# Kernel tuning notes

Measured on AMD Instinct MI355X. Metric: run time of the kernel, lower is better.

The kernel has to match this reference:

```python
import jax, jax.numpy as jnp
import numpy as np

BETA = 0.25  # cfg.vq_commitment


def setup_inputs() -> dict:
    key = jax.random.key(0)
    k1, k2 = jax.random.split(key)
    residual = jax.random.normal(k1, (16, 2048, 512), dtype=jnp.float32)
    emb_weight = jax.random.normal(k2, (1024, 512), dtype=jnp.float32) * 0.02
    return {"residual": residual, "emb_weight": emb_weight}


def reference(residual, emb_weight):
    # Euclidean branch (vq_cosine=False), no factorized projection (rvq_code_dim<=0)
    r = residual                                     # [B, T, D]
    z2 = jnp.sum(r * r, axis=-1, keepdims=True)      # [B, T, 1]
    e2 = jnp.sum(emb_weight * emb_weight, axis=-1)   # [N]
    # dist[b,t,n] = ||r_bt||^2 + ||e_n||^2 - 2 <r_bt, e_n>
    dist = z2 + e2 - 2.0 * jnp.einsum('btd,nd->btn', r, emb_weight)
    idx = jnp.argmin(dist, axis=-1)                  # [B, T] int
    z_q = emb_weight[idx]                            # gather, [B, T, D]
    # straight-through estimator
    z_st = residual + jax.lax.stop_gradient(z_q - residual)
    commit = jnp.mean((jax.lax.stop_gradient(z_q) - residual) ** 2)
    codebook = jnp.mean((z_q - jax.lax.stop_gradient(residual)) ** 2)
    loss = BETA * commit + codebook
    return (z_st, loss, dist, idx)
```

## Files before the change

### kernel.cpp

```cpp
#include <hip/hip_runtime.h>
#include <cfloat>
#include <stdint.h>

#define D       512
#define NCODES  1024
#define MROWS   32768

#define ZST_OFF  0
#define LOSS_OFF 16777216
#define DIST_OFF 16777217ull
#define IDX_OFF  50331649

#define WS_Z2   524288
#define WS_E2   557056
#define WS_LOSS 558080

typedef __attribute__((ext_vector_type(4))) float f32x4;
typedef __attribute__((ext_vector_type(4))) int   i32x4;
typedef __bf16 bf16v8 __attribute__((ext_vector_type(8)));

static __device__ __forceinline__ uint32_t f2bf(float x) {
    uint32_t u = __float_as_uint(x);
    return (u + 0x7fffu + ((u >> 16) & 1u)) >> 16;
}
static __device__ __forceinline__ float bf2f(uint32_t h) {
    return __uint_as_float(h << 16);
}
static __device__ __forceinline__ f32x4 MFMA(bf16v8 a, bf16v8 b, f32x4 c) {
    return __builtin_amdgcn_mfma_f32_16x16x32_bf16(a, b, c, 0, 0, 0);
}

__global__ void prepass_kernel(const float* __restrict__ residual,
                               const float* __restrict__ emb,
                               float* __restrict__ ws,
                               float* __restrict__ out) {
    if (blockIdx.x == 0 && threadIdx.x == 0) ws[WS_LOSS] = 0.0f;
    const int gwave = (int)((blockIdx.x * blockDim.x + threadIdx.x) >> 6);
    const int lane  = threadIdx.x & 63;
    const bool isA  = gwave < MROWS;
    const float* src = isA ? residual + (size_t)gwave * D
                           : emb + (size_t)(gwave - MROWS) * D;
    const float4* vp = (const float4*)src;
    float4 x0 = vp[lane * 2];
    float4 x1 = vp[lane * 2 + 1];
    float xs[8] = {x0.x, x0.y, x0.z, x0.w, x1.x, x1.y, x1.z, x1.w};
    uint32_t hp[4], lp[4];
    float s = 0.f;
#pragma unroll
    for (int i = 0; i < 4; ++i) {
        float a = xs[2 * i], b = xs[2 * i + 1];
        s += a * a + b * b;
        uint32_t h0 = f2bf(a), h1 = f2bf(b);
        uint32_t l0 = f2bf(a - bf2f(h0)), l1 = f2bf(b - bf2f(h1));
        hp[i] = h0 | (h1 << 16);
        lp[i] = l0 | (l1 << 16);
    }
#pragma unroll
    for (int off = 32; off > 0; off >>= 1) s += __shfl_xor(s, off);

    const int kt = lane >> 3, c8 = lane & 7;
    i32x4 hv = {(int)hp[0], (int)hp[1], (int)hp[2], (int)hp[3]};
    i32x4 lv = {(int)lp[0], (int)lp[1], (int)lp[2], (int)lp[3]};
    if (isA) {
        const int bm = gwave >> 7, rl = gwave & 127;
        char* dst = (char*)out + (size_t)bm * 262144 + (size_t)kt * 32768
                  + rl * 128 + ((c8 * 16) ^ ((rl & 7) << 4));
        *(i32x4*)dst = hv;
        *(i32x4*)(dst + 16384) = lv;
        if (lane == 0) ws[WS_Z2 + gwave] = s;
    } else {
        const int n = gwave - MROWS, nt = n >> 8, cl = n & 255;
        char* dst = (char*)ws + (size_t)nt * 524288 + (size_t)kt * 65536
                  + cl * 128 + ((c8 * 16) ^ ((cl & 7) << 4));
        *(i32x4*)dst = hv;
        *(i32x4*)(dst + 32768) = lv;
        if (lane == 0) ws[WS_E2 + n] = s;
    }
}

__launch_bounds__(512, 2)
__global__ void vq_main_kernel(const float* __restrict__ residual,
                               const float* __restrict__ emb,
                               float* __restrict__ ws,
                               float* __restrict__ out) {
    __shared__ __align__(16) char smem[98304];
    const int tid  = threadIdx.x;
    const int wid  = tid >> 6, lane = tid & 63;
    const int ln15 = lane & 15, kg = lane >> 4;
    const int wm   = wid >> 2, wn = wid & 3;
    const int bm   = blockIdx.x;
    const int row0 = bm * 128;

    float z2r[16];
#pragma unroll
    for (int mf = 0; mf < 4; ++mf)
#pragma unroll
        for (int j = 0; j < 4; ++j)
            z2r[mf * 4 + j] = ws[WS_Z2 + row0 + wm * 64 + mf * 16 + kg * 4 + j];

    float runv[16];
    int   runi[16];
#pragma unroll
    for (int li = 0; li < 16; ++li) { runv[li] = FLT_MAX; runi[li] = 0; }

    int aoff[4][2], boff[4][2];
#pragma unroll
    for (int mf = 0; mf < 4; ++mf) {
        const int rA = wm * 64 + mf * 16 + ln15;
#pragma unroll
        for (int ks = 0; ks < 2; ++ks)
            aoff[mf][ks] = rA * 128 + ((ks * 64 + kg * 16) ^ ((rA & 7) << 4));
    }
#pragma unroll
    for (int nf = 0; nf < 4; ++nf) {
        const int cB = wn * 64 + nf * 16 + ln15;
#pragma unroll
        for (int ks = 0; ks < 2; ++ks)
            boff[nf][ks] = 32768 + cB * 128 + ((ks * 64 + kg * 16) ^ ((cB & 7) << 4));
    }

    const char* srcA = (const char*)out + (size_t)bm * 262144;
    const char* srcB = (const char*)ws;

    for (int nt = 0; nt < 4; ++nt) {
        f32x4 acc[4][4];
#pragma unroll
        for (int mf = 0; mf < 4; ++mf)
#pragma unroll
            for (int nf = 0; nf < 4; ++nf) acc[mf][nf] = 0.f;

        for (int kt = 0; kt < 8; ++kt) {
            __syncthreads();
            {
                const char* ga = srcA + (size_t)kt * 32768 + wid * 1024 + lane * 16;
                char* la = smem + wid * 1024;
#pragma unroll
                for (int i = 0; i < 4; ++i)
                    __builtin_amdgcn_global_load_lds((const uint32_t*)(ga + i * 8192),
                                                     (uint32_t*)(la + i * 8192), 16, 0, 0);
                const char* gb = srcB + (size_t)nt * 524288 + (size_t)kt * 65536
                               + wid * 1024 + lane * 16;
                char* lb = smem + 32768 + wid * 1024;
#pragma unroll
                for (int i = 0; i < 8; ++i)
                    __builtin_amdgcn_global_load_lds((const uint32_t*)(gb + i * 8192),
                                                     (uint32_t*)(lb + i * 8192), 16, 0, 0);
            }
            __syncthreads();

#pragma unroll
            for (int ks = 0; ks < 2; ++ks) {
                bf16v8 ah[4], al[4], bh[4], bl[4];
#pragma unroll
                for (int mf = 0; mf < 4; ++mf) {
                    ah[mf] = *(const bf16v8*)(smem + aoff[mf][ks]);
                    al[mf] = *(const bf16v8*)(smem + aoff[mf][ks] + 16384);
                }
#pragma unroll
                for (int nf = 0; nf < 4; ++nf) {
                    bh[nf] = *(const bf16v8*)(smem + boff[nf][ks]);
                    bl[nf] = *(const bf16v8*)(smem + boff[nf][ks] + 32768);
                }
#pragma unroll
                for (int mf = 0; mf < 4; ++mf)
#pragma unroll
                    for (int nf = 0; nf < 4; ++nf) {
                        acc[mf][nf] = MFMA(ah[mf], bh[nf], acc[mf][nf]);
                        acc[mf][nf] = MFMA(ah[mf], bl[nf], acc[mf][nf]);
                        acc[mf][nf] = MFMA(al[mf], bh[nf], acc[mf][nf]);
                    }
            }
        }

        float e2v[4];
#pragma unroll
        for (int nf = 0; nf < 4; ++nf)
            e2v[nf] = ws[WS_E2 + nt * 256 + wn * 64 + nf * 16 + ln15];
#pragma unroll
        for (int mf = 0; mf < 4; ++mf)
#pragma unroll
            for (int nf = 0; nf < 4; ++nf)
#pragma unroll
                for (int j = 0; j < 4; ++j) {
                    const float dv = (z2r[mf * 4 + j] + e2v[nf]) - 2.0f * acc[mf][nf][j];
                    const int grow = row0 + wm * 64 + mf * 16 + kg * 4 + j;
                    const int gcol = nt * 256 + wn * 64 + nf * 16 + ln15;
                    out[DIST_OFF + (size_t)grow * 1024 + gcol] = dv;
                    const int li = mf * 4 + j;
                    if (dv < runv[li]) { runv[li] = dv; runi[li] = gcol; }
                }
    }

#pragma unroll
    for (int off = 1; off < 16; off <<= 1) {
#pragma unroll
        for (int li = 0; li < 16; ++li) {
            const float ov = __shfl_xor(runv[li], off);
            const int   oi = __shfl_xor(runi[li], off);
            if (ov < runv[li] || (ov == runv[li] && oi < runi[li])) {
                runv[li] = ov; runi[li] = oi;
            }
        }
    }

    float* smin = (float*)smem;
    int*   sidx = (int*)(smem + 2048);
    int*   srowcode = (int*)(smem + 4096);
    float* swsum = (float*)(smem + 4608);
    __syncthreads();
    if (ln15 == 0) {
#pragma unroll
        for (int mf = 0; mf < 4; ++mf)
#pragma unroll
            for (int j = 0; j < 4; ++j) {
                const int rl = wm * 64 + mf * 16 + kg * 4 + j;
                smin[rl * 4 + wn] = runv[mf * 4 + j];
                sidx[rl * 4 + wn] = runi[mf * 4 + j];
            }
    }
    __syncthreads();
    if (tid < 128) {
        float bv = smin[tid * 4];
        int   bi = sidx[tid * 4];
#pragma unroll
        for (int c = 1; c < 4; ++c) {
            const float v  = smin[tid * 4 + c];
            const int   ci = sidx[tid * 4 + c];
            if (v < bv || (v == bv && ci < bi)) { bv = v; bi = ci; }
        }
        srowcode[tid] = bi;
        out[IDX_OFF + row0 + tid] = (float)bi;
    }
    __syncthreads();

    float lsum = 0.0f;
    for (int e4 = tid; e4 < 128 * 128; e4 += 512) {
        const int rl = e4 >> 7, dq = e4 & 127;
        const size_t gi = (size_t)(row0 + rl) * D + dq * 4;
        float4 rv = *(const float4*)&residual[gi];
        const int code = srowcode[rl];
        float4 ev = *(const float4*)&emb[(size_t)code * D + dq * 4];
        float4 st;
        const float dx = ev.x - rv.x, dy = ev.y - rv.y;
        const float dz = ev.z - rv.z, dw = ev.w - rv.w;
        st.x = rv.x + dx; st.y = rv.y + dy; st.z = rv.z + dz; st.w = rv.w + dw;
        *(float4*)&out[ZST_OFF + gi] = st;
        lsum += dx * dx + dy * dy + dz * dz + dw * dw;
    }
#pragma unroll
    for (int off = 32; off > 0; off >>= 1) lsum += __shfl_xor(lsum, off);
    if (lane == 0) swsum[wid] = lsum;
    __syncthreads();
    if (tid == 0) {
        float s = 0.0f;
#pragma unroll
        for (int w = 0; w < 8; ++w) s += swsum[w];
        atomicAdd(&ws[WS_LOSS], s);
    }
}

__global__ void finalize_kernel(const float* __restrict__ ws,
                                float* __restrict__ out) {
    out[LOSS_OFF] = 1.25f * ws[WS_LOSS] / 16777216.0f;
}

extern "C" void kernel_launch(void* const* d_in, const int* in_sizes, int n_in,
                              void* d_out, int out_size, void* d_ws, size_t ws_size,
                              hipStream_t stream) {
    const float* residual = (const float*)d_in[0];
    const float* emb      = (const float*)d_in[1];
    float* out = (float*)d_out;
    float* ws  = (float*)d_ws;

    prepass_kernel<<<8448, 256, 0, stream>>>(residual, emb, ws, out);
    vq_main_kernel<<<MROWS / 128, 512, 0, stream>>>(residual, emb, ws, out);
    finalize_kernel<<<1, 1, 0, stream>>>(ws, out);
}
```

Measured before the change: 399.1 us.

## Double-buffer LDS staging with smaller K tiles and restructure prepass layout

The main GEMM loop now uses K tiles of 32 instead of 64, held in two LDS buffers, so the next tile's global-to-LDS load is issued while the current tile is computed. This removes one barrier per iteration and overlaps memory with MFMA work. The prepass is rewritten so each wave covers 16 rows by a 32-wide K slice with a new swizzle. Row norms are now accumulated by atomics into a zeroed workspace, and a separate kernel computes the codebook norms. The cost is more loop iterations, extra launches and a memset, and float atomics for z2 that make the summation order nondeterministic.

After: 455.8 us. 1.14x slower.

```diff
diff --git a/kernel.cpp b/kernel.cpp
--- a/kernel.cpp
+++ b/kernel.cpp
@@ -30,52 +30,72 @@
     return __builtin_amdgcn_mfma_f32_16x16x32_bf16(a, b, c, 0, 0, 0);
 }
 
+__global__ void e2_kernel(const float* __restrict__ emb,
+                          float* __restrict__ ws) {
+    const int gw   = (int)((blockIdx.x * blockDim.x + threadIdx.x) >> 6);
+    const int lane = threadIdx.x & 63;
+    const float4* v = (const float4*)(emb + (size_t)gw * D);
+    float4 a = v[lane * 2];
+    float4 b = v[lane * 2 + 1];
+    float s = a.x*a.x + a.y*a.y + a.z*a.z + a.w*a.w
+            + b.x*b.x + b.y*b.y + b.z*b.z + b.w*b.w;
+#pragma unroll
+    for (int off = 32; off > 0; off >>= 1) s += __shfl_xor(s, off);
+    if (lane == 0) ws[WS_E2 + gw] = s;
+}
+
 __global__ void prepass_kernel(const float* __restrict__ residual,
                                const float* __restrict__ emb,
                                float* __restrict__ ws,
                                float* __restrict__ out) {
-    if (blockIdx.x == 0 && threadIdx.x == 0) ws[WS_LOSS] = 0.0f;
     const int gwave = (int)((blockIdx.x * blockDim.x + threadIdx.x) >> 6);
     const int lane  = threadIdx.x & 63;
-    const bool isA  = gwave < MROWS;
-    const float* src = isA ? residual + (size_t)gwave * D
-                           : emb + (size_t)(gwave - MROWS) * D;
-    const float4* vp = (const float4*)src;
-    float4 x0 = vp[lane * 2];
-    float4 x1 = vp[lane * 2 + 1];
-    float xs[8] = {x0.x, x0.y, x0.z, x0.w, x1.x, x1.y, x1.z, x1.w};
+    const int rowgroup = gwave >> 4;
+    const int kt       = gwave & 15;
+    const int r = lane >> 2;
+    const int c = lane & 3;
+    const bool isA = rowgroup < (MROWS / 16);
+    const int gr = isA ? rowgroup * 16 + r : (rowgroup - MROWS / 16) * 16 + r;
+    const float* src = (isA ? residual : emb) + (size_t)gr * D + kt * 32 + c * 8;
+    const float4 x0 = ((const float4*)src)[0];
+    const float4 x1 = ((const float4*)src)[1];
+    const float xs[8] = {x0.x, x0.y, x0.z, x0.w, x1.x, x1.y, x1.z, x1.w};
     uint32_t hp[4], lp[4];
     float s = 0.f;
 #pragma unroll
     for (int i = 0; i < 4; ++i) {
-        float a = xs[2 * i], b = xs[2 * i + 1];
+        const float a = xs[2 * i], b = xs[2 * i + 1];
         s += a * a + b * b;
-        uint32_t h0 = f2bf(a), h1 = f2bf(b);
-        uint32_t l0 = f2bf(a - bf2f(h0)), l1 = f2bf(b - bf2f(h1));
+        const uint32_t h0 = f2bf(a), h1 = f2bf(b);
+        const uint32_t l0 = f2bf(a - bf2f(h0)), l1 = f2bf(b - bf2f(h1));
         hp[i] = h0 | (h1 << 16);
         lp[i] = l0 | (l1 << 16);
     }
-#pragma unroll
-    for (int off = 32; off > 0; off >>= 1) s += __shfl_xor(s, off);
-
-    const int kt = lane >> 3, c8 = lane & 7;
-    i32x4 hv = {(int)hp[0], (int)hp[1], (int)hp[2], (int)hp[3]};
-    i32x4 lv = {(int)lp[0], (int)lp[1], (int)lp[2], (int)lp[3]};
     if (isA) {
-        const int bm = gwave >> 7, rl = gwave & 127;
-        char* dst = (char*)out + (size_t)bm * 262144 + (size_t)kt * 32768
-                  + rl * 128 + ((c8 * 16) ^ ((rl & 7) << 4));
-        *(i32x4*)dst = hv;
-        *(i32x4*)(dst + 16384) = lv;
-        if (lane == 0) ws[WS_Z2 + gwave] = s;
+        float t = s;
+        t += __shfl_xor(t, 1);
+        t += __shfl_xor(t, 2);
+        if (c == 0) atomicAdd(&ws[WS_Z2 + gr], t);
+    }
+    const i32x4 hv = {(int)hp[0], (int)hp[1], (int)hp[2], (int)hp[3]};
+    const i32x4 lv = {(int)lp[0], (int)lp[1], (int)lp[2], (int)lp[3]};
+    char* dst;
+    int comp_stride;
+    if (isA) {
+        const int bm = gr >> 7, rl = gr & 127;
+        const int slot = c ^ ((rl >> 1) & 3);
+        dst = (char*)out + (size_t)bm * 262144 + (size_t)kt * 16384
+            + rl * 64 + slot * 16;
+        comp_stride = 8192;
     } else {
-        const int n = gwave - MROWS, nt = n >> 8, cl = n & 255;
-        char* dst = (char*)ws + (size_t)nt * 524288 + (size_t)kt * 65536
-                  + cl * 128 + ((c8 * 16) ^ ((cl & 7) << 4));
-        *(i32x4*)dst = hv;
-        *(i32x4*)(dst + 32768) = lv;
-        if (lane == 0) ws[WS_E2 + n] = s;
-    }
+        const int nt = gr >> 8, cl = gr & 255;
+        const int slot = c ^ ((cl >> 1) & 3);
+        dst = (char*)ws + (size_t)nt * 524288 + (size_t)kt * 32768
+            + cl * 64 + slot * 16;
+        comp_stride = 16384;
+    }
+    *(i32x4*)dst = hv;
+    *(i32x4*)(dst + comp_stride) = lv;
 }
 
 __launch_bounds__(512, 2)
@@ -91,6 +111,21 @@
     const int bm   = blockIdx.x;
     const int row0 = bm * 128;
 
+    const char* Aimg = (const char*)out + (size_t)bm * 262144;
+    const char* Bimg = (const char*)ws;
+
+    int aoff[4], boff[4];
+#pragma unroll
+    for (int mf = 0; mf < 4; ++mf) {
+        const int rA = wm * 64 + mf * 16 + ln15;
+        aoff[mf] = rA * 64 + 16 * (kg ^ ((rA >> 1) & 3));
+    }
+#pragma unroll
+    for (int nf = 0; nf < 4; ++nf) {
+        const int cB = wn * 64 + nf * 16 + ln15;
+        boff[nf] = 16384 + cB * 64 + 16 * (kg ^ ((cB >> 1) & 3));
+    }
+
     float z2r[16];
 #pragma unroll
     for (int mf = 0; mf < 4; ++mf)
@@ -103,24 +138,23 @@
 #pragma unroll
     for (int li = 0; li < 16; ++li) { runv[li] = FLT_MAX; runi[li] = 0; }
 
-    int aoff[4][2], boff[4][2];
-#pragma unroll
-    for (int mf = 0; mf < 4; ++mf) {
-        const int rA = wm * 64 + mf * 16 + ln15;
-#pragma unroll
-        for (int ks = 0; ks < 2; ++ks)
-            aoff[mf][ks] = rA * 128 + ((ks * 64 + kg * 16) ^ ((rA & 7) << 4));
-    }
-#pragma unroll
-    for (int nf = 0; nf < 4; ++nf) {
-        const int cB = wn * 64 + nf * 16 + ln15;
-#pragma unroll
-        for (int ks = 0; ks < 2; ++ks)
-            boff[nf][ks] = 32768 + cB * 128 + ((ks * 64 + kg * 16) ^ ((cB & 7) << 4));
-    }
-
-    const char* srcA = (const char*)out + (size_t)bm * 262144;
-    const char* srcB = (const char*)ws;
+    auto STAGE = [&](int s, char* buf) {
+        const int snt = s >> 4, skt = s & 15;
+        const char* ga = Aimg + (size_t)skt * 16384 + wid * 1024 + lane * 16;
+        char* la = buf + wid * 1024;
+        __builtin_amdgcn_global_load_lds((const uint32_t*)ga, (uint32_t*)la, 16, 0, 0);
+        __builtin_amdgcn_global_load_lds((const uint32_t*)(ga + 8192),
+                                         (uint32_t*)(la + 8192), 16, 0, 0);
+        const char* gb = Bimg + (size_t)snt * 524288 + (size_t)skt * 32768
+                       + wid * 1024 + lane * 16;
+        char* lb = buf + 16384 + wid * 1024;
+#pragma unroll
+        for (int i = 0; i < 4; ++i)
+            __builtin_amdgcn_global_load_lds((const uint32_t*)(gb + i * 8192),
+                                             (uint32_t*)(lb + i * 8192), 16, 0, 0);
+    };
+
+    STAGE(0, smem);
 
     for (int nt = 0; nt < 4; ++nt) {
         f32x4 acc[4][4];
@@ -129,66 +163,53 @@
 #pragma unroll
             for (int nf = 0; nf < 4; ++nf) acc[mf][nf] = 0.f;
 
-        for (int kt = 0; kt < 8; ++kt) {
+        for (int kt = 0; kt < 16; ++kt) {
+            const int s = nt * 16 + kt;
             __syncthreads();
-            {
-                const char* ga = srcA + (size_t)kt * 32768 + wid * 1024 + lane * 16;
-                char* la = smem + wid * 1024;
-#pragma unroll
-                for (int i = 0; i < 4; ++i)
-                    __builtin_amdgcn_global_load_lds((const uint32_t*)(ga + i * 8192),
-                                                     (uint32_t*)(la + i * 8192), 16, 0, 0);
-                const char* gb = srcB + (size_t)nt * 524288 + (size_t)kt * 65536
-                               + wid * 1024 + lane * 16;
-                char* lb = smem + 32768 + wid * 1024;
-#pragma unroll
-                for (int i = 0; i < 8; ++i)
-                    __builtin_amdgcn_global_load_lds((const uint32_t*)(gb + i * 8192),
-                                                     (uint32_t*)(lb + i * 8192), 16, 0, 0);
-            }
-            __syncthreads();
-
-#pragma unroll
-            for (int ks = 0; ks < 2; ++ks) {
-                bf16v8 ah[4], al[4], bh[4], bl[4];
-#pragma unroll
-                for (int mf = 0; mf < 4; ++mf) {
-                    ah[mf] = *(const bf16v8*)(smem + aoff[mf][ks]);
-                    al[mf] = *(const bf16v8*)(smem + aoff[mf][ks] + 16384);
+            if (s < 63) STAGE(s + 1, smem + ((s + 1) & 1) * 49152);
+            const char* buf = smem + (s & 1) * 49152;
+
+            bf16v8 ah[4], al[4], bh[4], bl[4];
+#pragma unroll
+            for (int mf = 0; mf < 4; ++mf) {
+                ah[mf] = *(const bf16v8*)(buf + aoff[mf]);
+                al[mf] = *(const bf16v8*)(buf + aoff[mf] + 8192);
+            }
+#pragma unroll
+            for (int nf = 0; nf < 4; ++nf) {
+                bh[nf] = *(const bf16v8*)(buf + boff[nf]);
+                bl[nf] = *(const bf16v8*)(buf + boff[nf] + 16384);
+            }
+#pragma unroll
+            for (int mf = 0; mf < 4; ++mf)
+#pragma unroll
+                for (int nf = 0; nf < 4; ++nf) {
+                    acc[mf][nf] = MFMA(ah[mf], bh[nf], acc[mf][nf]);
+                    acc[mf][nf] = MFMA(ah[mf], bl[nf], acc[mf][nf]);
+                    acc[mf][nf] = MFMA(al[mf], bh[nf], acc[mf][nf]);
                 }
-#pragma unroll
-                for (int nf = 0; nf < 4; ++nf) {
-                    bh[nf] = *(const bf16v8*)(smem + boff[nf][ks]);
-                    bl[nf] = *(const bf16v8*)(smem + boff[nf][ks] + 32768);
-                }
+
+            if (kt == 15) {
+                float e2v[4];
+#pragma unroll
+                for (int nf = 0; nf < 4; ++nf)
+                    e2v[nf] = ws[WS_E2 + nt * 256 + wn * 64 + nf * 16 + ln15];
 #pragma unroll
                 for (int mf = 0; mf < 4; ++mf)
 #pragma unroll
-                    for (int nf = 0; nf < 4; ++nf) {
-                        acc[mf][nf] = MFMA(ah[mf], bh[nf], acc[mf][nf]);
-                        acc[mf][nf] = MFMA(ah[mf], bl[nf], acc[mf][nf]);
-                        acc[mf][nf] = MFMA(al[mf], bh[nf], acc[mf][nf]);
-                    }
+                    for (int nf = 0; nf < 4; ++nf)
+#pragma unroll
+                        for (int j = 0; j < 4; ++j) {
+                            const float dv = (z2r[mf * 4 + j] + e2v[nf])
+                                           - 2.0f * acc[mf][nf][j];
+                            const int grow = row0 + wm * 64 + mf * 16 + kg * 4 + j;
+                            const int gcol = nt * 256 + wn * 64 + nf * 16 + ln15;
+                            out[DIST_OFF + (size_t)grow * 1024 + gcol] = dv;
+                            const int li = mf * 4 + j;
+                            if (dv < runv[li]) { runv[li] = dv; runi[li] = gcol; }
+                        }
             }
         }
-
-        float e2v[4];
-#pragma unroll
-        for (int nf = 0; nf < 4; ++nf)
-            e2v[nf] = ws[WS_E2 + nt * 256 + wn * 64 + nf * 16 + ln15];
-#pragma unroll
-        for (int mf = 0; mf < 4; ++mf)
-#pragma unroll
-            for (int nf = 0; nf < 4; ++nf)
-#pragma unroll
-                for (int j = 0; j < 4; ++j) {
-                    const float dv = (z2r[mf * 4 + j] + e2v[nf]) - 2.0f * acc[mf][nf][j];
-                    const int grow = row0 + wm * 64 + mf * 16 + kg * 4 + j;
-                    const int gcol = nt * 256 + wn * 64 + nf * 16 + ln15;
-                    out[DIST_OFF + (size_t)grow * 1024 + gcol] = dv;
-                    const int li = mf * 4 + j;
-                    if (dv < runv[li]) { runv[li] = dv; runi[li] = gcol; }
-                }
     }
 
 #pragma unroll
@@ -237,9 +258,9 @@
     for (int e4 = tid; e4 < 128 * 128; e4 += 512) {
         const int rl = e4 >> 7, dq = e4 & 127;
         const size_t gi = (size_t)(row0 + rl) * D + dq * 4;
-        float4 rv = *(const float4*)&residual[gi];
+        const float4 rv = *(const float4*)&residual[gi];
         const int code = srowcode[rl];
-        float4 ev = *(const float4*)&emb[(size_t)code * D + dq * 4];
+        const float4 ev = *(const float4*)&emb[(size_t)code * D + dq * 4];
         float4 st;
         const float dx = ev.x - rv.x, dy = ev.y - rv.y;
         const float dz = ev.z - rv.z, dw = ev.w - rv.w;
@@ -252,10 +273,10 @@
     if (lane == 0) swsum[wid] = lsum;
     __syncthreads();
     if (tid == 0) {
-        float s = 0.0f;
-#pragma unroll
-        for (int w = 0; w < 8; ++w) s += swsum[w];
-        atomicAdd(&ws[WS_LOSS], s);
+        float ssum = 0.0f;
+#pragma unroll
+        for (int w = 0; w < 8; ++w) ssum += swsum[w];
+        atomicAdd(&ws[WS_LOSS], ssum);
     }
 }
 
@@ -272,7 +293,10 @@
     float* out = (float*)d_out;
     float* ws  = (float*)d_ws;
 
+    hipMemsetAsync((char*)d_ws + (size_t)WS_Z2 * 4, 0,
+                   (size_t)(MROWS + NCODES + 1) * 4, stream);
     prepass_kernel<<<8448, 256, 0, stream>>>(residual, emb, ws, out);
+    e2_kernel<<<256, 256, 0, stream>>>(emb, ws);
     vq_main_kernel<<<MROWS / 128, 512, 0, stream>>>(residual, emb, ws, out);
     finalize_kernel<<<1, 1, 0, stream>>>(ws, out);
 }
```
